# Kernel optimization log

Hardware: AMD Instinct MI355X
Metric: run time of the kernel (lower is better)

Reference implementation:

```python
import jax, jax.numpy as jnp
import numpy as np
from jax import lax

ALPHA = 50.0
BN_EPS = 1e-5
L2_EPS = 1e-12

N, C, H, W = 32, 128, 128, 128
K = 64  # num_clusters


def _l2norm(v, axis):
    n = jnp.sqrt(jnp.sum(v * v, axis=axis, keepdims=True))
    return v / jnp.maximum(n, L2_EPS)


def setup_inputs() -> dict:
    key = jax.random.key(0)
    ks = jax.random.split(key, 4)
    x = jax.random.normal(ks[0], (N, C, H, W), dtype=jnp.float32)
    conv_w = jax.random.normal(ks[1], (C, C, 3, 3), dtype=jnp.float32) * 0.05
    bn_gamma = jnp.ones((C,), jnp.float32)
    bn_beta = jnp.zeros((C,), jnp.float32)
    bn_mean = jnp.zeros((C,), jnp.float32)
    bn_var = jnp.ones((C,), jnp.float32)
    # conv.weight in NetVLAD is centroids.permute(1,0): shape (dim, num_clusters)
    vlad_w = jax.random.normal(ks[2], (C, K), dtype=jnp.float32)
    vlad_b = jnp.zeros((K,), jnp.float32)  # initialized to zeros in _init_params
    return {"input": x, "conv_w": conv_w, "bn_gamma": bn_gamma, "bn_beta": bn_beta,
            "bn_mean": bn_mean, "bn_var": bn_var, "vlad_w": vlad_w, "vlad_b": vlad_b,
            "norm_flag": 1}


def reference(input, conv_w, bn_gamma, bn_beta, bn_mean, bn_var, vlad_w, vlad_b, norm_flag):
    # bottleneck_layer_2: conv3x3 stride2 pad1 (no bias) -> BN (eval form) -> ReLU
    f = lax.conv_general_dilated(input, conv_w, window_strides=(2, 2),
                                 padding=[(1, 1), (1, 1)],
                                 dimension_numbers=("NCHW", "OIHW", "NCHW"))
    inv = bn_gamma / jnp.sqrt(bn_var + BN_EPS)
    f = f * inv[None, :, None, None] + (bn_beta - bn_mean * inv)[None, :, None, None]
    f = jax.nn.relu(f)

    n, c, h, w = f.shape
    hw = h * w
    # normalize_input: L2 over channel dim
    xn = _l2norm(f, axis=1)
    xf = xn.reshape(n, c, hw)  # (N,C,HW)

    # soft assignment: x^T @ normalize(W, dim=0), bias added, softmax over clusters
    wn = _l2norm(vlad_w, axis=0)                     # (C,K)
    sa_ = jnp.einsum("nci,ck->nik", xf, wn)          # (N,HW,K)
    logits = jnp.swapaxes(sa_, 1, 2) + vlad_b[None, :, None]  # (N,K,HW)
    a = jax.nn.softmax(ALPHA * logits, axis=1)       # softmax over K

    # vlad_k = sum_i a_ki * x_i - (sum_i a_ki) * c_k  (c_k = vlad_w[:,k], unnormalized)
    asum = jnp.sum(a, axis=-1)                       # (N,K)
    vlad = jnp.einsum("nki,nci->nkc", a, xf) - asum[:, :, None] * vlad_w.T[None]  # (N,K,C)

    vlad = _l2norm(vlad, axis=2)                     # intra-normalization
    vlad = vlad.reshape(n, -1)
    vlad = _l2norm(vlad, axis=1)

    feature = jnp.swapaxes(xf, 1, 2)                 # (N,HW,C)
    soft_assign_out = jnp.swapaxes(sa_, 1, 2)        # (N,K,HW)
    return (vlad, soft_assign_out, feature)
```

## Files before the change

### kernel.cpp

```cpp
#include <hip/hip_runtime.h>

typedef short short8 __attribute__((ext_vector_type(8)));
typedef float floatx4 __attribute__((ext_vector_type(4)));

#define ALPHA 50.0f
#define BN_EPS 1e-5f

#define SA_BASE   262144L
#define FEAT_BASE 8650752L

#define T_OFF    0L
#define PART_OFF 138444800L
#define WB_OFF   171999232L
#define WNA_OFF  172294144L
#define ASUM_OFF 172310528L

__device__ __forceinline__ unsigned short f2bf(float f) {
    unsigned u = __builtin_bit_cast(unsigned, f);
    u = u + 0x7FFFu + ((u >> 16) & 1u);
    return (unsigned short)(u >> 16);
}

__device__ __forceinline__ void gl_lds16(const void* g, void* l) {
    __builtin_amdgcn_global_load_lds(
        (const __attribute__((address_space(1))) unsigned int*)g,
        (__attribute__((address_space(3))) unsigned int*)l, 16, 0, 0);
}

__global__ __launch_bounds__(256) void k_prep(const float* __restrict__ conv_w,
                                              const float* __restrict__ vlad_w,
                                              unsigned short* __restrict__ wB,
                                              unsigned short* __restrict__ wnA,
                                              float* __restrict__ asum) {
    int b = blockIdx.x, t = threadIdx.x;
    if (b < 576) {
        int idx = b * 256 + t;
        int ci = idx & 127, co = (idx >> 7) & 127, tap = idx >> 14;
        float w = conv_w[(co * 128 + ci) * 9 + tap];
        wB[(tap * 128 + co) * 128 + ci] = f2bf(w);
    } else {
        if (t < 64) {
            int k = t;
            float s = 0.0f;
            for (int c = 0; c < 128; c++) { float w = vlad_w[c * 64 + k]; s += w * w; }
            float rs = 1.0f / fmaxf(sqrtf(s), 1e-12f);
            for (int c = 0; c < 128; c++) wnA[k * 128 + c] = f2bf(vlad_w[c * 64 + k] * rs);
        } else {
            for (int i = t - 64; i < 2048; i += 192) asum[i] = 0.0f;
        }
    }
}

__global__ __launch_bounds__(256) void k_border(unsigned short* __restrict__ T) {
    int n = blockIdx.x, t = threadIdx.x;
    uint4 z = make_uint4(0, 0, 0, 0);
    for (int i = t; i < 4128; i += 256) {
        long e;
        if (i < 2080) {
            int ix = i >> 4, oct = i & 15;
            e = (((long)n * 130 + 0) * 130 + ix) * 128 + oct * 8;
        } else {
            int j = i - 2080;
            int row = (j >> 4) + 1, oct = j & 15;
            e = (((long)n * 130 + row) * 130 + 0) * 128 + oct * 8;
        }
        *(uint4*)(T + e) = z;
    }
}

__global__ __launch_bounds__(256) void k_xform(const float* __restrict__ in,
                                               unsigned short* __restrict__ T) {
    int y = blockIdx.x, n = blockIdx.y, t = threadIdx.x;
    __shared__ float ls[64 * 133];
    for (int cc = 0; cc < 2; cc++) {
        __syncthreads();
        int ci0 = cc * 64;
#pragma unroll
        for (int i = 0; i < 8; i++) {
            int idx = i * 256 + t;
            int ci = idx >> 5, xq = idx & 31;
            float4 v = *(const float4*)(in + ((((long)n * 128 + ci0 + ci) * 128 + y) * 128 + xq * 4));
            *(float4*)(&ls[ci * 133 + xq * 4]) = v;
        }
        __syncthreads();
#pragma unroll
        for (int i = 0; i < 4; i++) {
            int idx = i * 256 + t;
            int x = idx >> 3, oct = idx & 7;
            short8 pk;
#pragma unroll
            for (int j = 0; j < 8; j++)
                pk[j] = (short)f2bf(ls[(oct * 8 + j) * 133 + x]);
            long e = (((long)n * 130 + y + 1) * 130 + (x + 1)) * 128 + ci0 + oct * 8;
            *(short8*)(T + e) = pk;
        }
    }
}

__global__ __launch_bounds__(256) void k_conv(const unsigned short* __restrict__ T,
                                              const unsigned short* __restrict__ wB,
                                              const float* __restrict__ gamma,
                                              const float* __restrict__ beta,
                                              const float* __restrict__ mean,
                                              const float* __restrict__ var,
                                              const unsigned short* __restrict__ wnA,
                                              const float* __restrict__ vlad_b,
                                              float* __restrict__ out,
                                              float* __restrict__ part,
                                              float* __restrict__ asum) {
    int ypair = blockIdx.x, n = blockIdx.y;
    int t = threadIdx.x, lane = t & 63, w = t >> 6;
    int wm = w >> 1, wn = w & 1;
    int s = lane & 15, q = lane >> 4;
    int y0 = ypair * 2;

    __shared__ __align__(16) short lsA[26112];
    __shared__ float lsq[256];

    floatx4 acc[4][4];
#pragma unroll
    for (int a = 0; a < 4; a++)
#pragma unroll
        for (int b = 0; b < 4; b++) acc[a][b] = (floatx4){0.f, 0.f, 0.f, 0.f};

    const unsigned short* Tbase = T + (((long)n * 130 + 2 * y0) * 130) * 128;
    int bbase0 = (wn * 64 + s) * 128 + q * 8;

    for (int cc = 0; cc < 4; cc++) {
        int ci0 = cc * 32;
        const unsigned short* Tc = Tbase + ci0;
#pragma unroll
        for (int i = 0; i < 11; i++) {
            int f = i * 256 + t;
            short* lbase = &lsA[2048 * i + 512 * w];
            if (f < 2600) {
                int r = f / 520;
                int rem = f - r * 520;
                int p = rem >> 3;
                int o8 = (rem & 7) ^ (p & 7);
                int ix = 2 * p + (o8 >> 2);
                int oct = o8 & 3;
                gl_lds16(Tc + (((long)(r * 130 + ix)) << 7) + (oct << 3), lbase);
            }
        }
        __syncthreads();
#pragma unroll
        for (int tap = 0; tap < 9; tap++) {
            const int dy = tap / 3, dx = tap % 3;
            short8 af[4], bf[4];
#pragma unroll
            for (int tm = 0; tm < 4; tm++) {
                int x = tm * 16 + s;
                int p = x + (dx >> 1);
                int o8p = (((dx & 1) << 2) | q) ^ (p & 7);
                int r = 2 * wm + dy;
                af[tm] = *(const short8*)(&lsA[(((r * 65 + p) << 3) + o8p) << 3]);
            }
#pragma unroll
            for (int tn = 0; tn < 4; tn++)
                bf[tn] = *(const short8*)(wB + bbase0 + tap * 16384 + tn * 2048 + ci0);
#pragma unroll
            for (int tm = 0; tm < 4; tm++)
#pragma unroll
                for (int tn = 0; tn < 4; tn++)
                    acc[tm][tn] = __builtin_amdgcn_mfma_f32_16x16x32_bf16(af[tm], bf[tn], acc[tm][tn], 0, 0, 0);
        }
        __syncthreads();
    }

    float inv[4], bt[4];
#pragma unroll
    for (int tn = 0; tn < 4; tn++) {
        int co = wn * 64 + tn * 16 + s;
        inv[tn] = gamma[co] / sqrtf(var[co] + BN_EPS);
        bt[tn] = beta[co] - mean[co] * inv[tn];
    }
#pragma unroll
    for (int tm = 0; tm < 4; tm++)
#pragma unroll
        for (int tn = 0; tn < 4; tn++)
#pragma unroll
            for (int r = 0; r < 4; r++) {
                float f = acc[tm][tn][r] * inv[tn] + bt[tn];
                acc[tm][tn][r] = fmaxf(f, 0.0f);
            }
#pragma unroll
    for (int tm = 0; tm < 4; tm++)
#pragma unroll
        for (int r = 0; r < 4; r++) {
            float p = 0.f;
#pragma unroll
            for (int tn = 0; tn < 4; tn++) { float f = acc[tm][tn][r]; p += f * f; }
            p += __shfl_xor(p, 1); p += __shfl_xor(p, 2);
            p += __shfl_xor(p, 4); p += __shfl_xor(p, 8);
            if (s == 0) lsq[wn * 128 + wm * 64 + tm * 16 + q * 4 + r] = p;
        }
    __syncthreads();
    float scl[4][4];
#pragma unroll
    for (int tm = 0; tm < 4; tm++)
#pragma unroll
        for (int r = 0; r < 4; r++) {
            int m = wm * 64 + tm * 16 + q * 4 + r;
            float tot = lsq[m] + lsq[128 + m];
            scl[tm][r] = 1.0f / fmaxf(sqrtf(tot), 1e-12f);
        }
    short* lsT = lsA;
    long pixbase = (long)n * 4096 + y0 * 64;
#pragma unroll
    for (int tm = 0; tm < 4; tm++)
#pragma unroll
        for (int r = 0; r < 4; r++) {
            int m = wm * 64 + tm * 16 + q * 4 + r;
#pragma unroll
            for (int tn = 0; tn < 4; tn++) {
                int co = wn * 64 + tn * 16 + s;
                float xv = acc[tm][tn][r] * scl[tm][r];
                out[FEAT_BASE + (pixbase + m) * 128 + co] = xv;
                lsT[co * 136 + m] = (short)f2bf(xv);
            }
        }
    __syncthreads();

    floatx4 acc2[4][2];
#pragma unroll
    for (int a = 0; a < 4; a++)
#pragma unroll
        for (int b = 0; b < 2; b++) acc2[a][b] = (floatx4){0.f, 0.f, 0.f, 0.f};
    int pixw = w * 32;
#pragma unroll
    for (int kk = 0; kk < 4; kk++) {
        int c0 = kk * 32 + q * 8;
        short8 af2[4], bf2[2];
#pragma unroll
        for (int tm = 0; tm < 4; tm++)
            af2[tm] = *(const short8*)(wnA + (tm * 16 + s) * 128 + c0);
#pragma unroll
        for (int tn = 0; tn < 2; tn++) {
            int pix = pixw + tn * 16 + s;
            short8 bv;
#pragma unroll
            for (int j = 0; j < 8; j++)
                bv[j] = lsT[(c0 + j) * 136 + pix];
            bf2[tn] = bv;
        }
#pragma unroll
        for (int tm = 0; tm < 4; tm++)
#pragma unroll
            for (int tn = 0; tn < 2; tn++)
                acc2[tm][tn] = __builtin_amdgcn_mfma_f32_16x16x32_bf16(af2[tm], bf2[tn], acc2[tm][tn], 0, 0, 0);
    }
    long sabase = SA_BASE + (long)n * 262144 + (long)(y0 * 64 + pixw);
#pragma unroll
    for (int tm = 0; tm < 4; tm++)
#pragma unroll
        for (int r = 0; r < 4; r++) {
            int k = tm * 16 + q * 4 + r;
#pragma unroll
            for (int tn = 0; tn < 2; tn++)
                out[sabase + (long)k * 4096 + tn * 16 + s] = acc2[tm][tn][r];
        }
    float bv2[4][4];
#pragma unroll
    for (int tm = 0; tm < 4; tm++)
#pragma unroll
        for (int r = 0; r < 4; r++) bv2[tm][r] = vlad_b[tm * 16 + q * 4 + r];
#pragma unroll
    for (int tn = 0; tn < 2; tn++) {
        float M = -1e30f;
#pragma unroll
        for (int tm = 0; tm < 4; tm++)
#pragma unroll
            for (int r = 0; r < 4; r++)
                M = fmaxf(M, ALPHA * (acc2[tm][tn][r] + bv2[tm][r]));
        M = fmaxf(M, __shfl_xor(M, 16)); M = fmaxf(M, __shfl_xor(M, 32));
        float S = 0.f;
#pragma unroll
        for (int tm = 0; tm < 4; tm++)
#pragma unroll
            for (int r = 0; r < 4; r++) {
                float p = expf(ALPHA * (acc2[tm][tn][r] + bv2[tm][r]) - M);
                acc2[tm][tn][r] = p; S += p;
            }
        S += __shfl_xor(S, 16); S += __shfl_xor(S, 32);
        float rS = 1.0f / S;
#pragma unroll
        for (int tm = 0; tm < 4; tm++)
#pragma unroll
            for (int r = 0; r < 4; r++) acc2[tm][tn][r] *= rS;
    }
    short* lsAa = lsA + 17408;
#pragma unroll
    for (int tm = 0; tm < 4; tm++)
#pragma unroll
        for (int r = 0; r < 4; r++) {
            int k = tm * 16 + q * 4 + r;
#pragma unroll
            for (int tn = 0; tn < 2; tn++)
                lsAa[k * 136 + pixw + tn * 16 + s] = (short)f2bf(acc2[tm][tn][r]);
            float p = acc2[tm][0][r] + acc2[tm][1][r];
            p += __shfl_xor(p, 1); p += __shfl_xor(p, 2);
            p += __shfl_xor(p, 4); p += __shfl_xor(p, 8);
            if (s == 0) atomicAdd(asum + n * 64 + k, p);
        }
    __syncthreads();
    floatx4 acc3[2][4];
#pragma unroll
    for (int a = 0; a < 2; a++)
#pragma unroll
        for (int b = 0; b < 4; b++) acc3[a][b] = (floatx4){0.f, 0.f, 0.f, 0.f};
    int kh = (w >> 1) * 32, ch0 = (w & 1) * 64;
#pragma unroll
    for (int pc = 0; pc < 4; pc++) {
        int p0 = pc * 32 + q * 8;
        short8 aA[2], bB[4];
#pragma unroll
        for (int tk = 0; tk < 2; tk++)
            aA[tk] = *(const short8*)(lsAa + (kh + tk * 16 + s) * 136 + p0);
#pragma unroll
        for (int tc = 0; tc < 4; tc++)
            bB[tc] = *(const short8*)(lsT + (ch0 + tc * 16 + s) * 136 + p0);
#pragma unroll
        for (int tk = 0; tk < 2; tk++)
#pragma unroll
            for (int tc = 0; tc < 4; tc++)
                acc3[tk][tc] = __builtin_amdgcn_mfma_f32_16x16x32_bf16(aA[tk], bB[tc], acc3[tk][tc], 0, 0, 0);
    }
    float* pp = part + ((long)n * 32 + ypair) * 8192;
#pragma unroll
    for (int tk = 0; tk < 2; tk++)
#pragma unroll
        for (int r = 0; r < 4; r++) {
            int k = kh + tk * 16 + q * 4 + r;
#pragma unroll
            for (int tc = 0; tc < 4; tc++)
                pp[k * 128 + ch0 + tc * 16 + s] = acc3[tk][tc][r];
        }
}

__global__ __launch_bounds__(256) void k_vlad2(const float* __restrict__ part,
                                               const float* __restrict__ vlad_w,
                                               const float* __restrict__ asum,
                                               float* __restrict__ out) {
    int n = blockIdx.x;
    int t = threadIdx.x, lane = t & 63, w = t >> 6;
    __shared__ float lsq[128];
    __shared__ float gsq[4];

    float v[32];
    const float* pb = part + (long)n * 32 * 8192;
#pragma unroll
    for (int j = 0; j < 32; j++) {
        int e = j * 256 + t;
        float sacc = 0.f;
#pragma unroll 8
        for (int c8 = 0; c8 < 32; c8++) sacc += pb[c8 * 8192 + e];
        int k = e >> 7, c = e & 127;
        sacc -= asum[n * 64 + k] * vlad_w[c * 64 + k];
        v[j] = sacc;
        float p = sacc * sacc;
        p += __shfl_xor(p, 1); p += __shfl_xor(p, 2); p += __shfl_xor(p, 4);
        p += __shfl_xor(p, 8); p += __shfl_xor(p, 16); p += __shfl_xor(p, 32);
        if (lane == 0) lsq[j * 4 + w] = p;
    }
    __syncthreads();
    float gp = 0.f;
#pragma unroll
    for (int j = 0; j < 32; j++) {
        float tot = lsq[j * 4 + (w & 2)] + lsq[j * 4 + (w & 2) + 1];
        float sc = 1.0f / fmaxf(sqrtf(tot), 1e-12f);
        v[j] *= sc;
        gp += v[j] * v[j];
    }
    gp += __shfl_xor(gp, 1); gp += __shfl_xor(gp, 2); gp += __shfl_xor(gp, 4);
    gp += __shfl_xor(gp, 8); gp += __shfl_xor(gp, 16); gp += __shfl_xor(gp, 32);
    if (lane == 0) gsq[w] = gp;
    __syncthreads();
    float sc2 = 1.0f / fmaxf(sqrtf(gsq[0] + gsq[1] + gsq[2] + gsq[3]), 1e-12f);
#pragma unroll
    for (int j = 0; j < 32; j++)
        out[(long)n * 8192 + j * 256 + t] = v[j] * sc2;
}

extern "C" void kernel_launch(void* const* d_in, const int* in_sizes, int n_in,
                              void* d_out, int out_size, void* d_ws, size_t ws_size,
                              hipStream_t stream) {
    const float* input  = (const float*)d_in[0];
    const float* conv_w = (const float*)d_in[1];
    const float* gamma  = (const float*)d_in[2];
    const float* beta   = (const float*)d_in[3];
    const float* mean   = (const float*)d_in[4];
    const float* var    = (const float*)d_in[5];
    const float* vlad_w = (const float*)d_in[6];
    const float* vlad_b = (const float*)d_in[7];
    float* out = (float*)d_out;
    char* ws = (char*)d_ws;

    unsigned short* T   = (unsigned short*)(ws + T_OFF);
    float* part         = (float*)(ws + PART_OFF);
    unsigned short* wB  = (unsigned short*)(ws + WB_OFF);
    unsigned short* wnA = (unsigned short*)(ws + WNA_OFF);
    float* asum         = (float*)(ws + ASUM_OFF);

    k_prep<<<577, 256, 0, stream>>>(conv_w, vlad_w, wB, wnA, asum);
    k_border<<<32, 256, 0, stream>>>(T);
    k_xform<<<dim3(128, 32), 256, 0, stream>>>(input, T);
    k_conv<<<dim3(32, 32), 256, 0, stream>>>(T, wB, gamma, beta, mean, var, wnA, vlad_b, out, part, asum);
    k_vlad2<<<32, 256, 0, stream>>>(part, vlad_w, asum, out);
}
```

Before: 640.2 us.

## Shrink conv tile to one output row and accumulate VLAD via atomics

The fused conv/VLAD kernel now handles one output row per block instead of two, doubling the grid to 2048 blocks and roughly halving LDS use. This should raise occupancy and wave count on the GPU. Per-block VLAD partials are no longer written to a scratch buffer and reduced in k_vlad2; blocks atomically add into a zeroed per-image accumulator. asum atomics are first reduced across waves in LDS, cutting atomic traffic. In exchange, it adds float atomic contention on 8192 entries per image, non-deterministic summation order, and reloads the conv weights twice as often.

```diff
diff --git a/kernel.cpp b/kernel.cpp
--- a/kernel.cpp
+++ b/kernel.cpp
@@ -10,10 +10,10 @@
 #define FEAT_BASE 8650752L
 
 #define T_OFF    0L
-#define PART_OFF 138444800L
-#define WB_OFF   171999232L
-#define WNA_OFF  172294144L
-#define ASUM_OFF 172310528L
+#define WB_OFF   138444800L
+#define WNA_OFF  138739712L
+#define ASUM_OFF 138756096L
+#define VACC_OFF 138764288L
 
 __device__ __forceinline__ unsigned short f2bf(float f) {
     unsigned u = __builtin_bit_cast(unsigned, f);
@@ -30,28 +30,25 @@
 __global__ __launch_bounds__(256) void k_prep(const float* __restrict__ conv_w,
                                               const float* __restrict__ vlad_w,
                                               unsigned short* __restrict__ wB,
-                                              unsigned short* __restrict__ wnA,
-                                              float* __restrict__ asum) {
+                                              unsigned short* __restrict__ wnA) {
     int b = blockIdx.x, t = threadIdx.x;
     if (b < 576) {
         int idx = b * 256 + t;
         int ci = idx & 127, co = (idx >> 7) & 127, tap = idx >> 14;
         float w = conv_w[(co * 128 + ci) * 9 + tap];
         wB[(tap * 128 + co) * 128 + ci] = f2bf(w);
-    } else {
-        if (t < 64) {
-            int k = t;
-            float s = 0.0f;
-            for (int c = 0; c < 128; c++) { float w = vlad_w[c * 64 + k]; s += w * w; }
-            float rs = 1.0f / fmaxf(sqrtf(s), 1e-12f);
-            for (int c = 0; c < 128; c++) wnA[k * 128 + c] = f2bf(vlad_w[c * 64 + k] * rs);
-        } else {
-            for (int i = t - 64; i < 2048; i += 192) asum[i] = 0.0f;
-        }
-    }
-}
-
-__global__ __launch_bounds__(256) void k_border(unsigned short* __restrict__ T) {
+    } else if (t < 64) {
+        int k = t;
+        float s = 0.0f;
+        for (int c = 0; c < 128; c++) { float w = vlad_w[c * 64 + k]; s += w * w; }
+        float rs = 1.0f / fmaxf(sqrtf(s), 1e-12f);
+        for (int c = 0; c < 128; c++) wnA[k * 128 + c] = f2bf(vlad_w[c * 64 + k] * rs);
+    }
+}
+
+__global__ __launch_bounds__(256) void k_border(unsigned short* __restrict__ T,
+                                                float* __restrict__ vacc,
+                                                float* __restrict__ asum) {
     int n = blockIdx.x, t = threadIdx.x;
     uint4 z = make_uint4(0, 0, 0, 0);
     for (int i = t; i < 4128; i += 256) {
@@ -66,6 +63,10 @@
         }
         *(uint4*)(T + e) = z;
     }
+    float4 zf = make_float4(0.f, 0.f, 0.f, 0.f);
+    for (int i = t; i < 2048; i += 256)
+        *(float4*)(vacc + (long)n * 8192 + i * 4) = zf;
+    if (t < 64) asum[n * 64 + t] = 0.0f;
 }
 
 __global__ __launch_bounds__(256) void k_xform(const float* __restrict__ in,
@@ -106,34 +107,33 @@
                                               const unsigned short* __restrict__ wnA,
                                               const float* __restrict__ vlad_b,
                                               float* __restrict__ out,
-                                              float* __restrict__ part,
+                                              float* __restrict__ vacc,
                                               float* __restrict__ asum) {
-    int ypair = blockIdx.x, n = blockIdx.y;
+    int y = blockIdx.x, n = blockIdx.y;
     int t = threadIdx.x, lane = t & 63, w = t >> 6;
     int wm = w >> 1, wn = w & 1;
     int s = lane & 15, q = lane >> 4;
-    int y0 = ypair * 2;
-
-    __shared__ __align__(16) short lsA[26112];
+
+    __shared__ __align__(16) short lsA[13824];
     __shared__ float lsq[256];
 
-    floatx4 acc[4][4];
-#pragma unroll
-    for (int a = 0; a < 4; a++)
+    floatx4 acc[2][4];
+#pragma unroll
+    for (int a = 0; a < 2; a++)
 #pragma unroll
         for (int b = 0; b < 4; b++) acc[a][b] = (floatx4){0.f, 0.f, 0.f, 0.f};
 
-    const unsigned short* Tbase = T + (((long)n * 130 + 2 * y0) * 130) * 128;
+    const unsigned short* Tbase = T + (((long)n * 130 + 2 * y) * 130) * 128;
     int bbase0 = (wn * 64 + s) * 128 + q * 8;
 
     for (int cc = 0; cc < 4; cc++) {
         int ci0 = cc * 32;
         const unsigned short* Tc = Tbase + ci0;
 #pragma unroll
-        for (int i = 0; i < 11; i++) {
+        for (int i = 0; i < 7; i++) {
             int f = i * 256 + t;
             short* lbase = &lsA[2048 * i + 512 * w];
-            if (f < 2600) {
+            if (f < 1560) {
                 int r = f / 520;
                 int rem = f - r * 520;
                 int p = rem >> 3;
@@ -147,20 +147,19 @@
 #pragma unroll
         for (int tap = 0; tap < 9; tap++) {
             const int dy = tap / 3, dx = tap % 3;
-            short8 af[4], bf[4];
-#pragma unroll
-            for (int tm = 0; tm < 4; tm++) {
-                int x = tm * 16 + s;
+            short8 af[2], bf[4];
+#pragma unroll
+            for (int tm = 0; tm < 2; tm++) {
+                int x = wm * 32 + tm * 16 + s;
                 int p = x + (dx >> 1);
                 int o8p = (((dx & 1) << 2) | q) ^ (p & 7);
-                int r = 2 * wm + dy;
-                af[tm] = *(const short8*)(&lsA[(((r * 65 + p) << 3) + o8p) << 3]);
+                af[tm] = *(const short8*)(&lsA[(((dy * 65 + p) << 3) + o8p) << 3]);
             }
 #pragma unroll
             for (int tn = 0; tn < 4; tn++)
                 bf[tn] = *(const short8*)(wB + bbase0 + tap * 16384 + tn * 2048 + ci0);
 #pragma unroll
-            for (int tm = 0; tm < 4; tm++)
+            for (int tm = 0; tm < 2; tm++)
 #pragma unroll
                 for (int tn = 0; tn < 4; tn++)
                     acc[tm][tn] = __builtin_amdgcn_mfma_f32_16x16x32_bf16(af[tm], bf[tn], acc[tm][tn], 0, 0, 0);
@@ -176,7 +175,7 @@
         bt[tn] = beta[co] - mean[co] * inv[tn];
     }
 #pragma unroll
-    for (int tm = 0; tm < 4; tm++)
+    for (int tm = 0; tm < 2; tm++)
 #pragma unroll
         for (int tn = 0; tn < 4; tn++)
 #pragma unroll
@@ -185,7 +184,7 @@
                 acc[tm][tn][r] = fmaxf(f, 0.0f);
             }
 #pragma unroll
-    for (int tm = 0; tm < 4; tm++)
+    for (int tm = 0; tm < 2; tm++)
 #pragma unroll
         for (int r = 0; r < 4; r++) {
             float p = 0.f;
@@ -193,117 +192,104 @@
             for (int tn = 0; tn < 4; tn++) { float f = acc[tm][tn][r]; p += f * f; }
             p += __shfl_xor(p, 1); p += __shfl_xor(p, 2);
             p += __shfl_xor(p, 4); p += __shfl_xor(p, 8);
-            if (s == 0) lsq[wn * 128 + wm * 64 + tm * 16 + q * 4 + r] = p;
-        }
-    __syncthreads();
-    float scl[4][4];
-#pragma unroll
-    for (int tm = 0; tm < 4; tm++)
-#pragma unroll
-        for (int r = 0; r < 4; r++) {
-            int m = wm * 64 + tm * 16 + q * 4 + r;
-            float tot = lsq[m] + lsq[128 + m];
+            if (s == 0) lsq[wn * 64 + wm * 32 + tm * 16 + q * 4 + r] = p;
+        }
+    __syncthreads();
+    float scl[2][4];
+#pragma unroll
+    for (int tm = 0; tm < 2; tm++)
+#pragma unroll
+        for (int r = 0; r < 4; r++) {
+            int m = wm * 32 + tm * 16 + q * 4 + r;
+            float tot = lsq[m] + lsq[64 + m];
             scl[tm][r] = 1.0f / fmaxf(sqrtf(tot), 1e-12f);
         }
     short* lsT = lsA;
-    long pixbase = (long)n * 4096 + y0 * 64;
-#pragma unroll
-    for (int tm = 0; tm < 4; tm++)
-#pragma unroll
-        for (int r = 0; r < 4; r++) {
-            int m = wm * 64 + tm * 16 + q * 4 + r;
+    long pixbase = (long)n * 4096 + y * 64;
+#pragma unroll
+    for (int tm = 0; tm < 2; tm++)
+#pragma unroll
+        for (int r = 0; r < 4; r++) {
+            int m = wm * 32 + tm * 16 + q * 4 + r;
 #pragma unroll
             for (int tn = 0; tn < 4; tn++) {
                 int co = wn * 64 + tn * 16 + s;
                 float xv = acc[tm][tn][r] * scl[tm][r];
                 out[FEAT_BASE + (pixbase + m) * 128 + co] = xv;
-                lsT[co * 136 + m] = (short)f2bf(xv);
+                lsT[co * 72 + m] = (short)f2bf(xv);
             }
         }
     __syncthreads();
 
-    floatx4 acc2[4][2];
-#pragma unroll
-    for (int a = 0; a < 4; a++)
-#pragma unroll
-        for (int b = 0; b < 2; b++) acc2[a][b] = (floatx4){0.f, 0.f, 0.f, 0.f};
-    int pixw = w * 32;
+    floatx4 acc2[4];
+#pragma unroll
+    for (int a = 0; a < 4; a++) acc2[a] = (floatx4){0.f, 0.f, 0.f, 0.f};
+    int pixw = w * 16;
 #pragma unroll
     for (int kk = 0; kk < 4; kk++) {
         int c0 = kk * 32 + q * 8;
-        short8 af2[4], bf2[2];
+        short8 af2[4], bf2;
 #pragma unroll
         for (int tm = 0; tm < 4; tm++)
             af2[tm] = *(const short8*)(wnA + (tm * 16 + s) * 128 + c0);
 #pragma unroll
-        for (int tn = 0; tn < 2; tn++) {
-            int pix = pixw + tn * 16 + s;
-            short8 bv;
-#pragma unroll
-            for (int j = 0; j < 8; j++)
-                bv[j] = lsT[(c0 + j) * 136 + pix];
-            bf2[tn] = bv;
-        }
+        for (int j = 0; j < 8; j++)
+            bf2[j] = lsT[(c0 + j) * 72 + pixw + s];
 #pragma unroll
         for (int tm = 0; tm < 4; tm++)
-#pragma unroll
-            for (int tn = 0; tn < 2; tn++)
-                acc2[tm][tn] = __builtin_amdgcn_mfma_f32_16x16x32_bf16(af2[tm], bf2[tn], acc2[tm][tn], 0, 0, 0);
-    }
-    long sabase = SA_BASE + (long)n * 262144 + (long)(y0 * 64 + pixw);
+            acc2[tm] = __builtin_amdgcn_mfma_f32_16x16x32_bf16(af2[tm], bf2, acc2[tm], 0, 0, 0);
+    }
+    long sabase = SA_BASE + (long)n * 262144 + y * 64 + pixw;
 #pragma unroll
     for (int tm = 0; tm < 4; tm++)
 #pragma unroll
         for (int r = 0; r < 4; r++) {
             int k = tm * 16 + q * 4 + r;
-#pragma unroll
-            for (int tn = 0; tn < 2; tn++)
-                out[sabase + (long)k * 4096 + tn * 16 + s] = acc2[tm][tn][r];
+            out[sabase + (long)k * 4096 + s] = acc2[tm][r];
         }
     float bv2[4][4];
 #pragma unroll
     for (int tm = 0; tm < 4; tm++)
 #pragma unroll
         for (int r = 0; r < 4; r++) bv2[tm][r] = vlad_b[tm * 16 + q * 4 + r];
-#pragma unroll
-    for (int tn = 0; tn < 2; tn++) {
-        float M = -1e30f;
-#pragma unroll
-        for (int tm = 0; tm < 4; tm++)
-#pragma unroll
-            for (int r = 0; r < 4; r++)
-                M = fmaxf(M, ALPHA * (acc2[tm][tn][r] + bv2[tm][r]));
-        M = fmaxf(M, __shfl_xor(M, 16)); M = fmaxf(M, __shfl_xor(M, 32));
-        float S = 0.f;
-#pragma unroll
-        for (int tm = 0; tm < 4; tm++)
-#pragma unroll
-            for (int r = 0; r < 4; r++) {
-                float p = expf(ALPHA * (acc2[tm][tn][r] + bv2[tm][r]) - M);
-                acc2[tm][tn][r] = p; S += p;
-            }
-        S += __shfl_xor(S, 16); S += __shfl_xor(S, 32);
-        float rS = 1.0f / S;
-#pragma unroll
-        for (int tm = 0; tm < 4; tm++)
-#pragma unroll
-            for (int r = 0; r < 4; r++) acc2[tm][tn][r] *= rS;
-    }
-    short* lsAa = lsA + 17408;
+    float M = -1e30f;
+#pragma unroll
+    for (int tm = 0; tm < 4; tm++)
+#pragma unroll
+        for (int r = 0; r < 4; r++)
+            M = fmaxf(M, ALPHA * (acc2[tm][r] + bv2[tm][r]));
+    M = fmaxf(M, __shfl_xor(M, 16)); M = fmaxf(M, __shfl_xor(M, 32));
+    float S = 0.f;
+#pragma unroll
+    for (int tm = 0; tm < 4; tm++)
+#pragma unroll
+        for (int r = 0; r < 4; r++) {
+            float p = expf(ALPHA * (acc2[tm][r] + bv2[tm][r]) - M);
+            acc2[tm][r] = p; S += p;
+        }
+    S += __shfl_xor(S, 16); S += __shfl_xor(S, 32);
+    float rS = 1.0f / S;
+#pragma unroll
+    for (int tm = 0; tm < 4; tm++)
+#pragma unroll
+        for (int r = 0; r < 4; r++) acc2[tm][r] *= rS;
+    short* lsAa = lsA + 9216;
 #pragma unroll
     for (int tm = 0; tm < 4; tm++)
 #pragma unroll
         for (int r = 0; r < 4; r++) {
             int k = tm * 16 + q * 4 + r;
-#pragma unroll
-            for (int tn = 0; tn < 2; tn++)
-                lsAa[k * 136 + pixw + tn * 16 + s] = (short)f2bf(acc2[tm][tn][r]);
-            float p = acc2[tm][0][r] + acc2[tm][1][r];
+            lsAa[k * 72 + pixw + s] = (short)f2bf(acc2[tm][r]);
+            float p = acc2[tm][r];
             p += __shfl_xor(p, 1); p += __shfl_xor(p, 2);
             p += __shfl_xor(p, 4); p += __shfl_xor(p, 8);
-            if (s == 0) atomicAdd(asum + n * 64 + k, p);
-        }
-    __syncthreads();
+            if (s == 0) lsq[w * 64 + k] = p;
+        }
+    __syncthreads();
+    if (t < 64) {
+        float s4 = lsq[t] + lsq[64 + t] + lsq[128 + t] + lsq[192 + t];
+        atomicAdd(asum + n * 64 + t, s4);
+    }
     floatx4 acc3[2][4];
 #pragma unroll
     for (int a = 0; a < 2; a++)
@@ -311,22 +297,22 @@
         for (int b = 0; b < 4; b++) acc3[a][b] = (floatx4){0.f, 0.f, 0.f, 0.f};
     int kh = (w >> 1) * 32, ch0 = (w & 1) * 64;
 #pragma unroll
-    for (int pc = 0; pc < 4; pc++) {
+    for (int pc = 0; pc < 2; pc++) {
         int p0 = pc * 32 + q * 8;
         short8 aA[2], bB[4];
 #pragma unroll
         for (int tk = 0; tk < 2; tk++)
-            aA[tk] = *(const short8*)(lsAa + (kh + tk * 16 + s) * 136 + p0);
+            aA[tk] = *(const short8*)(lsAa + (kh + tk * 16 + s) * 72 + p0);
 #pragma unroll
         for (int tc = 0; tc < 4; tc++)
-            bB[tc] = *(const short8*)(lsT + (ch0 + tc * 16 + s) * 136 + p0);
+            bB[tc] = *(const short8*)(lsT + (ch0 + tc * 16 + s) * 72 + p0);
 #pragma unroll
         for (int tk = 0; tk < 2; tk++)
 #pragma unroll
             for (int tc = 0; tc < 4; tc++)
                 acc3[tk][tc] = __builtin_amdgcn_mfma_f32_16x16x32_bf16(aA[tk], bB[tc], acc3[tk][tc], 0, 0, 0);
     }
-    float* pp = part + ((long)n * 32 + ypair) * 8192;
+    float* vb = vacc + (long)n * 8192;
 #pragma unroll
     for (int tk = 0; tk < 2; tk++)
 #pragma unroll
@@ -334,11 +320,11 @@
             int k = kh + tk * 16 + q * 4 + r;
 #pragma unroll
             for (int tc = 0; tc < 4; tc++)
-                pp[k * 128 + ch0 + tc * 16 + s] = acc3[tk][tc][r];
-        }
-}
-
-__global__ __launch_bounds__(256) void k_vlad2(const float* __restrict__ part,
+                atomicAdd(vb + k * 128 + ch0 + tc * 16 + s, acc3[tk][tc][r]);
+        }
+}
+
+__global__ __launch_bounds__(256) void k_vlad2(const float* __restrict__ vacc,
                                                const float* __restrict__ vlad_w,
                                                const float* __restrict__ asum,
                                                float* __restrict__ out) {
@@ -348,15 +334,12 @@
     __shared__ float gsq[4];
 
     float v[32];
-    const float* pb = part + (long)n * 32 * 8192;
+    const float* vb = vacc + (long)n * 8192;
 #pragma unroll
     for (int j = 0; j < 32; j++) {
         int e = j * 256 + t;
-        float sacc = 0.f;
-#pragma unroll 8
-        for (int c8 = 0; c8 < 32; c8++) sacc += pb[c8 * 8192 + e];
         int k = e >> 7, c = e & 127;
-        sacc -= asum[n * 64 + k] * vlad_w[c * 64 + k];
+        float sacc = vb[e] - asum[n * 64 + k] * vlad_w[c * 64 + k];
         v[j] = sacc;
         float p = sacc * sacc;
         p += __shfl_xor(p, 1); p += __shfl_xor(p, 2); p += __shfl_xor(p, 4);
@@ -397,14 +380,14 @@
     char* ws = (char*)d_ws;
 
     unsigned short* T   = (unsigned short*)(ws + T_OFF);
-    float* part         = (float*)(ws + PART_OFF);
     unsigned short* wB  = (unsigned short*)(ws + WB_OFF);
     unsigned short* wnA = (unsigned short*)(ws + WNA_OFF);
     float* asum         = (float*)(ws + ASUM_OFF);
-
-    k_prep<<<577, 256, 0, stream>>>(conv_w, vlad_w, wB, wnA, asum);
-    k_border<<<32, 256, 0, stream>>>(T);
+    float* vacc         = (float*)(ws + VACC_OFF);
+
+    k_prep<<<577, 256, 0, stream>>>(conv_w, vlad_w, wB, wnA);
+    k_border<<<32, 256, 0, stream>>>(T, vacc, asum);
     k_xform<<<dim3(128, 32), 256, 0, stream>>>(input, T);
-    k_conv<<<dim3(32, 32), 256, 0, stream>>>(T, wB, gamma, beta, mean, var, wnA, vlad_b, out, part, asum);
-    k_vlad2<<<32, 256, 0, stream>>>(part, vlad_w, asum, out);
-}
+    k_conv<<<dim3(64, 32), 256, 0, stream>>>(T, wB, gamma, beta, mean, var, wnA, vlad_b, out, vacc, asum);
+    k_vlad2<<<32, 256, 0, stream>>>(vacc, vlad_w, asum, out);
+}
```

After: 632.8 us. Within noise of the previous version (-1.2%).
